# Performance work log

Measured on AMD Instinct MI355X. Metric: run time of the kernel, lower is better.

## Reference

```python
import jax, jax.numpy as jnp
import numpy as np

NUM_RAYS = 262144   # 512x512 rays
LENGTH = 128        # path_length
NUM_LEAVES = 1048576
MAX_DIST = 1e10
EPS = 1e-10


def setup_inputs() -> dict:
    key = jax.random.key(0)
    k1, k2, k3 = jax.random.split(key, 3)
    # t_stops must be increasing along each ray
    t_stops = jnp.sort(jax.random.uniform(k1, (NUM_RAYS, LENGTH), jnp.float32, 0.0, 4.0), axis=-1)
    leaves = jax.random.randint(k2, (NUM_RAYS, LENGTH), 0, NUM_LEAVES, dtype=jnp.int64)
    logits = jax.random.normal(k3, (NUM_LEAVES,), jnp.float32) - 10.0  # init near -10 like the module
    return {"t_stops": t_stops, "leaves": leaves, "logits": logits}


def reference(t_stops, leaves, logits):
    num_rays, length = leaves.shape
    # gather per-sample opacity
    opacity = jax.nn.sigmoid(logits)[leaves]                      # [R, L]
    # segment lengths; last segment extends to "infinity"
    deltas = jnp.concatenate(
        [t_stops[:, 1:] - t_stops[:, :-1],
         jnp.full((num_rays, 1), MAX_DIST, dtype=t_stops.dtype)], axis=-1)
    alpha = 1.0 - jnp.exp(-(opacity * deltas))                    # [R, L]
    trans = jnp.minimum(1.0, 1.0 - alpha + EPS)
    # shift right: transmittance before first sample is 1
    trans = jnp.concatenate(
        [jnp.ones((num_rays, 1), dtype=alpha.dtype), trans[:, 1:]], axis=-1)
    weights = alpha * jnp.cumprod(trans, axis=-1)                 # [R, L]
    return weights.sum(axis=-1)                                   # [R]
```

## Files before the change

kernel.cpp:

```cpp
#include <hip/hip_runtime.h>
#include <math.h>


#define NRAYS 262144
#define LEN   128
#define MAXD  1e10f
#define EPSW  1e-10f

__global__ __launch_bounds__(256) void vc_kernel(
    const float* __restrict__ t_stops,
    const int*   __restrict__ leaves,
    const float* __restrict__ logits,
    float*       __restrict__ out)
{
    const int lane = threadIdx.x & 63;
    const int wave = threadIdx.x >> 6;
    const int ray  = blockIdx.x * 4 + wave;

    const long long base = (long long)ray * LEN + 2 * lane;

    float2 t2 = *(const float2*)(t_stops + base);
    int2   lv = *(const int2*)(leaves + base);

    float t_next = __shfl_down(t2.x, 1);
    float d0 = t2.y - t2.x;
    float d1 = (lane == 63) ? MAXD : (t_next - t2.y);

    float lg0 = logits[lv.x];
    float lg1 = logits[lv.y];
    float op0 = 1.0f / (1.0f + expf(-lg0));
    float op1 = 1.0f / (1.0f + expf(-lg1));

    float a0 = -expm1f(-op0 * d0);
    float a1 = -expm1f(-op1 * d1);

    float tr0 = fminf(1.0f, 1.0f - a0 + EPSW);
    float tr1 = fminf(1.0f, 1.0f - a1 + EPSW);
    if (lane == 0) tr0 = 1.0f;

    float p01 = tr0 * tr1;

    float scan = p01;
    #pragma unroll
    for (int off = 1; off < 64; off <<= 1) {
        float v = __shfl_up(scan, off);
        if (lane >= off) scan *= v;
    }
    float excl = __shfl_up(scan, 1);
    if (lane == 0) excl = 1.0f;

    float w = a0 * (excl * tr0) + a1 * (excl * p01);

    #pragma unroll
    for (int off = 32; off >= 1; off >>= 1)
        w += __shfl_xor(w, off);

    if (lane == 0)
        out[ray] = w;
}

extern "C" void kernel_launch(void* const* d_in, const int* in_sizes, int n_in,
                              void* d_out, int out_size, void* d_ws, size_t ws_size,
                              hipStream_t stream) {
    const float* t_stops = (const float*)d_in[0];
    const int*   leaves  = (const int*)d_in[1];
    const float* logits  = (const float*)d_in[2];
    float*       out     = (float*)d_out;

    dim3 grid(NRAYS / 4), block(256);
    vc_kernel<<<grid, block, 0, stream>>>(t_stops, leaves, logits, out);
}
```

Measured before the change: 424.4 us.

## Precompute fp16 sigmoid table, give each lane 8 samples, use an associative segmented reduction

A pre-pass writes sigmoid(logits) as an fp16 table into workspace, which halves the bytes moved by the random gather and removes the per-sample sigmoid. The main kernel now processes four rays per wave with 16 lanes per ray and 8 samples per lane. It loads inputs with 128-bit nontemporal loads, forms the weighted sum serially within each lane, and combines lanes with an associative (product, sum) butterfly instead of a full-wave scan followed by a reduction. It also swaps the exact math for fast exp/rcp intrinsics and a polynomial for 1-exp(-x), which costs some precision and may move results off the fp32 reference.

```diff
diff --git a/kernel.cpp b/kernel.cpp
--- a/kernel.cpp
+++ b/kernel.cpp
@@ -1,62 +1,116 @@
 #include <hip/hip_runtime.h>
+#include <hip/hip_fp16.h>
 #include <math.h>
 
 
 #define NRAYS 262144
 #define LEN   128
+#define NLEAF 1048576
 #define MAXD  1e10f
 #define EPSW  1e-10f
 
+typedef float v4f __attribute__((ext_vector_type(4)));
+typedef int   v4i __attribute__((ext_vector_type(4)));
+
+__device__ __forceinline__ float fast_sigmoid(float x) {
+    return __builtin_amdgcn_rcpf(1.0f + __expf(-x));
+}
+
+__device__ __forceinline__ float omexp(float x) {
+    float p = x * (1.0f + x * (-0.5f + x * (0.16666667f - 0.041666668f * x)));
+    return (x < 0.1f) ? p : (1.0f - __expf(-x));
+}
+
+__global__ __launch_bounds__(256) void sig_kernel(const float* __restrict__ logits,
+                                                  __half* __restrict__ tab) {
+    int i = blockIdx.x * 256 + threadIdx.x;
+    tab[i] = __float2half(fast_sigmoid(logits[i]));
+}
+
+template <bool TAB>
 __global__ __launch_bounds__(256) void vc_kernel(
     const float* __restrict__ t_stops,
     const int*   __restrict__ leaves,
-    const float* __restrict__ logits,
+    const void*  __restrict__ table,
     float*       __restrict__ out)
 {
     const int lane = threadIdx.x & 63;
-    const int wave = threadIdx.x >> 6;
-    const int ray  = blockIdx.x * 4 + wave;
+    const int wid  = blockIdx.x * 4 + (threadIdx.x >> 6);
+    const int ray  = wid * 4 + (lane >> 4);
+    const int sub  = lane & 15;
 
-    const long long base = (long long)ray * LEN + 2 * lane;
+    const long long b0 = (long long)ray * LEN + sub * 4;
+    const long long b1 = b0 + 64;
 
-    float2 t2 = *(const float2*)(t_stops + base);
-    int2   lv = *(const int2*)(leaves + base);
+    v4i l0 = __builtin_nontemporal_load((const v4i*)(leaves + b0));
+    v4i l1 = __builtin_nontemporal_load((const v4i*)(leaves + b1));
+    v4f t0 = __builtin_nontemporal_load((const v4f*)(t_stops + b0));
+    v4f t1 = __builtin_nontemporal_load((const v4f*)(t_stops + b1));
 
-    float t_next = __shfl_down(t2.x, 1);
-    float d0 = t2.y - t2.x;
-    float d1 = (lane == 63) ? MAXD : (t_next - t2.y);
+    float op0, op1, op2, op3, op4, op5, op6, op7;
+    if (TAB) {
+        const __half* tb = (const __half*)table;
+        op0 = __half2float(tb[l0.x]);  op1 = __half2float(tb[l0.y]);
+        op2 = __half2float(tb[l0.z]);  op3 = __half2float(tb[l0.w]);
+        op4 = __half2float(tb[l1.x]);  op5 = __half2float(tb[l1.y]);
+        op6 = __half2float(tb[l1.z]);  op7 = __half2float(tb[l1.w]);
+    } else {
+        const float* lg = (const float*)table;
+        op0 = fast_sigmoid(lg[l0.x]);  op1 = fast_sigmoid(lg[l0.y]);
+        op2 = fast_sigmoid(lg[l0.z]);  op3 = fast_sigmoid(lg[l0.w]);
+        op4 = fast_sigmoid(lg[l1.x]);  op5 = fast_sigmoid(lg[l1.y]);
+        op6 = fast_sigmoid(lg[l1.z]);  op7 = fast_sigmoid(lg[l1.w]);
+    }
 
-    float lg0 = logits[lv.x];
-    float lg1 = logits[lv.y];
-    float op0 = 1.0f / (1.0f + expf(-lg0));
-    float op1 = 1.0f / (1.0f + expf(-lg1));
+    float tn0  = __shfl_down(t0.x, 1);
+    float tn1  = __shfl_down(t1.x, 1);
+    float tb1x = __shfl(t1.x, lane & 48);
 
-    float a0 = -expm1f(-op0 * d0);
-    float a1 = -expm1f(-op1 * d1);
+    float d0a = t0.y - t0.x, d0b = t0.z - t0.y, d0c = t0.w - t0.z;
+    float d0d = (sub == 15) ? (tb1x - t0.w) : (tn0 - t0.w);
+    float d1a = t1.y - t1.x, d1b = t1.z - t1.y, d1c = t1.w - t1.z;
+    float d1d = (sub == 15) ? MAXD : (tn1 - t1.w);
 
-    float tr0 = fminf(1.0f, 1.0f - a0 + EPSW);
-    float tr1 = fminf(1.0f, 1.0f - a1 + EPSW);
-    if (lane == 0) tr0 = 1.0f;
+    float a0 = omexp(op0 * d0a), a1 = omexp(op1 * d0b);
+    float a2 = omexp(op2 * d0c), a3 = omexp(op3 * d0d);
+    float a4 = omexp(op4 * d1a), a5 = omexp(op5 * d1b);
+    float a6 = omexp(op6 * d1c), a7 = omexp(op7 * d1d);
 
-    float p01 = tr0 * tr1;
+    float r0 = fminf(1.0f, 1.0f - a0 + EPSW), r1 = fminf(1.0f, 1.0f - a1 + EPSW);
+    float r2 = fminf(1.0f, 1.0f - a2 + EPSW), r3 = fminf(1.0f, 1.0f - a3 + EPSW);
+    float r4 = fminf(1.0f, 1.0f - a4 + EPSW), r5 = fminf(1.0f, 1.0f - a5 + EPSW);
+    float r6 = fminf(1.0f, 1.0f - a6 + EPSW), r7 = fminf(1.0f, 1.0f - a7 + EPSW);
+    if (sub == 0) r0 = 1.0f;
 
-    float scan = p01;
-    #pragma unroll
-    for (int off = 1; off < 64; off <<= 1) {
-        float v = __shfl_up(scan, off);
-        if (lane >= off) scan *= v;
-    }
-    float excl = __shfl_up(scan, 1);
-    if (lane == 0) excl = 1.0f;
-
-    float w = a0 * (excl * tr0) + a1 * (excl * p01);
+    float c0 = r0;            float S0 = a0 * c0;
+    c0 *= r1;                 S0 = fmaf(a1, c0, S0);
+    c0 *= r2;                 S0 = fmaf(a2, c0, S0);
+    c0 *= r3;                 S0 = fmaf(a3, c0, S0);
+    float P0 = c0;
+    float c1 = r4;            float S1 = a4 * c1;
+    c1 *= r5;                 S1 = fmaf(a5, c1, S1);
+    c1 *= r6;                 S1 = fmaf(a6, c1, S1);
+    c1 *= r7;                 S1 = fmaf(a7, c1, S1);
+    float P1 = c1;
 
     #pragma unroll
-    for (int off = 32; off >= 1; off >>= 1)
-        w += __shfl_xor(w, off);
+    for (int o = 1; o < 16; o <<= 1) {
+        float Pp0 = __shfl_xor(P0, o), Sp0 = __shfl_xor(S0, o);
+        float Pp1 = __shfl_xor(P1, o), Sp1 = __shfl_xor(S1, o);
+        if (lane & o) {
+            S0 = fmaf(Pp0, S0, Sp0);
+            S1 = fmaf(Pp1, S1, Sp1);
+        } else {
+            S0 = fmaf(P0, Sp0, S0);
+            S1 = fmaf(P1, Sp1, S1);
+        }
+        P0 *= Pp0;
+        P1 *= Pp1;
+    }
 
-    if (lane == 0)
-        out[ray] = w;
+    float S = fmaf(P0, S1, S0);
+    if (sub == 0)
+        out[ray] = S;
 }
 
 extern "C" void kernel_launch(void* const* d_in, const int* in_sizes, int n_in,
@@ -67,6 +121,10 @@
     const float* logits  = (const float*)d_in[2];
     float*       out     = (float*)d_out;
 
-    dim3 grid(NRAYS / 4), block(256);
-    vc_kernel<<<grid, block, 0, stream>>>(t_stops, leaves, logits, out);
+    if (ws_size >= NLEAF * sizeof(__half)) {
+        sig_kernel<<<NLEAF / 256, 256, 0, stream>>>(logits, (__half*)d_ws);
+        vc_kernel<true><<<NRAYS / 16, 256, 0, stream>>>(t_stops, leaves, d_ws, out);
+    } else {
+        vc_kernel<false><<<NRAYS / 16, 256, 0, stream>>>(t_stops, leaves, logits, out);
+    }
 }
```

Measured after the change: 371.6 us. 12.4% less time.
